# Kernel optimization log

Hardware: AMD Instinct MI355X
Metric: run time of the kernel (lower is better)

The kernel has to match this reference:

```python
import jax, jax.numpy as jnp
import numpy as np

D_MODEL = 1024
N_EXPERTS = 8
TOP_K = 2


def setup_inputs() -> dict:
    key = jax.random.key(0)
    ks = jax.random.split(key, 8)
    B, S, D, E, H = 4, 2048, D_MODEL, N_EXPERTS, 4 * D_MODEL
    s1 = 1.0 / np.sqrt(D)
    s2 = 1.0 / np.sqrt(H)
    return {
        "x": jax.random.normal(ks[0], (B, S, D), dtype=jnp.float32),
        "Wg": jax.random.uniform(ks[1], (D, E), jnp.float32, -s1, s1),
        "bg": jax.random.uniform(ks[2], (E,), jnp.float32, -s1, s1),
        "W1": jax.random.uniform(ks[3], (E, D, H), jnp.float32, -s1, s1),
        "b1": jax.random.uniform(ks[4], (E, H), jnp.float32, -s1, s1),
        "W2": jax.random.uniform(ks[5], (E, H, D), jnp.float32, -s2, s2),
        "b2": jax.random.uniform(ks[6], (E, D), jnp.float32, -s2, s2),
    }


def reference(x, Wg, bg, W1, b1, W2, b2):
    B, S, D = x.shape
    E = Wg.shape[1]
    x_flat = x.reshape(-1, D)                      # [T, D]
    logits = x_flat @ Wg + bg                      # [T, E]
    weights = jax.nn.softmax(logits, axis=-1)
    topk_w, topk_idx = jax.lax.top_k(weights, TOP_K)  # [T, K]
    # Per-token combine weight for each expert (sum over k where routed).
    onehot = jax.nn.one_hot(topk_idx, E, dtype=x.dtype)      # [T, K, E]
    combine = jnp.einsum("tk,tke->te", topk_w, onehot)       # [T, E]
    out = jnp.zeros_like(x_flat)
    for e in range(E):  # small fixed loop over experts
        h = jax.nn.gelu(x_flat @ W1[e] + b1[e], approximate=False)
        out = out + combine[:, e:e + 1] * (h @ W2[e] + b2[e])
    return out.reshape(B, S, D)
```

## Files before the change

### kernel.cpp

```cpp
#include <hip/hip_runtime.h>
#include <hip/hip_bf16.h>
#include <math.h>

#define T_TOK 8192
#define DM    1024
#define NE    8
#define HD    4096

typedef __bf16 bf16;
typedef __attribute__((ext_vector_type(8))) __bf16 bf16x8;
typedef __attribute__((ext_vector_type(4))) __bf16 bf16x4;
typedef __attribute__((ext_vector_type(4))) float  f32x4;

__device__ __forceinline__ void gl_lds16(const void* g, void* l) {
  __builtin_amdgcn_global_load_lds((const __attribute__((address_space(1))) void*)g,
                                   (__attribute__((address_space(3))) void*)l, 16, 0, 0);
}

#define RAW_BARRIER() asm volatile("s_barrier" ::: "memory")
#define WAIT_VM4()    asm volatile("s_waitcnt vmcnt(4)" ::: "memory")

__device__ __forceinline__ int imin(int a, int b) { return a < b ? a : b; }

__global__ void zero_kernel(float* __restrict__ out, int* __restrict__ counts) {
  size_t stride = (size_t)gridDim.x * blockDim.x;
  size_t n4 = (size_t)T_TOK * DM / 4;
  for (size_t i = (size_t)blockIdx.x * blockDim.x + threadIdx.x; i < n4; i += stride) {
    float4 z = {0.f, 0.f, 0.f, 0.f};
    ((float4*)out)[i] = z;
  }
  if (blockIdx.x == 0 && threadIdx.x < NE) counts[threadIdx.x] = 0;
}

__global__ void cvt_x_kernel(const float* __restrict__ x, bf16* __restrict__ xb) {
  size_t stride = (size_t)gridDim.x * blockDim.x;
  size_t n4 = (size_t)T_TOK * DM / 4;
  for (size_t i = (size_t)blockIdx.x * blockDim.x + threadIdx.x; i < n4; i += stride) {
    float4 v = ((const float4*)x)[i];
    bf16x4 o;
    o[0] = (bf16)v.x; o[1] = (bf16)v.y; o[2] = (bf16)v.z; o[3] = (bf16)v.w;
    *(bf16x4*)(xb + 4 * i) = o;
  }
}

__global__ void transpose_cvt_kernel(const float* __restrict__ in, bf16* __restrict__ out,
                                     int R, int C) {
  __shared__ float tile[64][65];
  int e = blockIdx.z;
  int c0 = blockIdx.x * 64, r0 = blockIdx.y * 64;
  int tid = threadIdx.x;
  int lr = tid >> 2, lc = (tid & 3) * 16;
  const float* src = in + ((size_t)e * R + r0 + lr) * C + c0 + lc;
#pragma unroll
  for (int q = 0; q < 4; ++q) {
    float4 v = *(const float4*)(src + q * 4);
    tile[lr][lc + q * 4 + 0] = v.x;
    tile[lr][lc + q * 4 + 1] = v.y;
    tile[lr][lc + q * 4 + 2] = v.z;
    tile[lr][lc + q * 4 + 3] = v.w;
  }
  __syncthreads();
  int oc = tid >> 3;
  int rchunk = tid & 7;
#pragma unroll
  for (int q = 0; q < 2; ++q) {
    int ocq = oc + q * 32;
    bf16x8 o;
#pragma unroll
    for (int k = 0; k < 8; ++k) o[k] = (bf16)tile[rchunk * 8 + k][ocq];
    *(bf16x8*)(out + ((size_t)e * C + c0 + ocq) * R + r0 + rchunk * 8) = o;
  }
}

__global__ void gating_kernel(const float* __restrict__ x, const float* __restrict__ Wg,
                              const float* __restrict__ bg, int* __restrict__ counts,
                              int* __restrict__ tokl, float* __restrict__ wgt) {
  int t = blockIdx.x * 4 + (threadIdx.x >> 6);
  int lane = threadIdx.x & 63;
  if (t >= T_TOK) return;
  double acc[NE];
#pragma unroll
  for (int e = 0; e < NE; ++e) acc[e] = 0.0;
  const float* xr = x + (size_t)t * DM;
  for (int d = lane; d < DM; d += 64) {
    float xv = xr[d];
#pragma unroll
    for (int e = 0; e < NE; ++e) acc[e] += (double)xv * (double)Wg[d * NE + e];
  }
#pragma unroll
  for (int e = 0; e < NE; ++e)
    for (int o = 32; o > 0; o >>= 1) acc[e] += __shfl_down(acc[e], o, 64);
  if (lane == 0) {
    float l[NE], w[NE];
    float m = -1e30f;
#pragma unroll
    for (int e = 0; e < NE; ++e) { l[e] = (float)acc[e] + bg[e]; m = fmaxf(m, l[e]); }
    float s = 0.f;
#pragma unroll
    for (int e = 0; e < NE; ++e) { w[e] = expf(l[e] - m); s += w[e]; }
    float inv = 1.f / s;
#pragma unroll
    for (int e = 0; e < NE; ++e) w[e] *= inv;
    int e1 = 0; float v1 = w[0];
#pragma unroll
    for (int e = 1; e < NE; ++e) if (w[e] > v1) { v1 = w[e]; e1 = e; }
    int e2 = -1; float v2 = -1.f;
#pragma unroll
    for (int e = 0; e < NE; ++e) if (e != e1 && w[e] > v2) { v2 = w[e]; e2 = e; }
    int s1 = atomicAdd(&counts[e1], 1);
    tokl[e1 * T_TOK + s1] = t; wgt[e1 * T_TOK + s1] = v1;
    int s2 = atomicAdd(&counts[e2], 1);
    tokl[e2 * T_TOK + s2] = t; wgt[e2 * T_TOK + s2] = v2;
  }
}

__global__ void scan_kernel(const int* __restrict__ counts, int* __restrict__ offsets) {
  if (threadIdx.x == 0 && blockIdx.x == 0) {
    int s = 0;
#pragma unroll
    for (int e = 0; e < NE; ++e) { offsets[e] = s; s += counts[e]; }
    offsets[NE] = s;
  }
}

__global__ __launch_bounds__(256, 3) void gemm1_kernel(
    const bf16* __restrict__ xbf, const bf16* __restrict__ w1t,
    const float* __restrict__ b1, const int* __restrict__ counts,
    const int* __restrict__ offsets, const int* __restrict__ tokl,
    bf16* __restrict__ hbuf, int Hc, int cbase) {
  int bid = blockIdx.x;
  int e = bid % NE;
  int pe = bid / NE;
  int NT = Hc / 128;
  int nt = pe % NT, rt = pe / NT;
  int cnt = counts[e];
  if (rt * 128 >= cnt) return;
  __shared__ __align__(16) bf16 sA[2][128 * 32];
  __shared__ __align__(16) bf16 sB[2][128 * 32];
  int tid = threadIdx.x, lane = tid & 63, w = tid >> 6;
  int slot = w * 2048 + lane * 16;
  int ra0 = slot >> 6, ko = slot & 63;
  int hoff = offsets[e];
  int r0 = imin(rt * 128 + ra0, cnt - 1);
  int r1 = imin(rt * 128 + ra0 + 16, cnt - 1);
  int t0 = tokl[e * T_TOK + r0];
  int t1 = tokl[e * T_TOK + r1];
  const char* ga0 = (const char*)(xbf + (size_t)t0 * DM) + ko;
  const char* ga1 = (const char*)(xbf + (size_t)t1 * DM) + ko;
  const char* gb0 = (const char*)(w1t + ((size_t)e * HD + cbase + nt * 128 + ra0) * DM) + ko;
  const char* gb1 = (const char*)(w1t + ((size_t)e * HD + cbase + nt * 128 + ra0 + 16) * DM) + ko;
  char* lab = (char*)sA + w * 2048;
  char* lbb = (char*)sB + w * 2048;
  f32x4 acc[4][4];
#pragma unroll
  for (int i = 0; i < 4; ++i)
#pragma unroll
    for (int j = 0; j < 4; ++j) acc[i][j] = {0.f, 0.f, 0.f, 0.f};
  int mw = (w & 1) * 64, nw = (w >> 1) * 64;
  const bf16* pa = &sA[0][0] + (size_t)(mw + (lane & 15)) * 32 + (lane >> 4) * 8;
  const bf16* pb = &sB[0][0] + (size_t)(nw + (lane & 15)) * 32 + (lane >> 4) * 8;
  const int K = DM / 32;
  gl_lds16(ga0, lab);
  gl_lds16(ga1, lab + 1024);
  gl_lds16(gb0, lbb);
  gl_lds16(gb1, lbb + 1024);
  for (int k = 0; k < K; ++k) {
    int nb = (k + 1) & 1;
    int kb = (k + 1 < K) ? (k + 1) * 64 : 0;
    gl_lds16(ga0 + kb, lab + nb * 8192);
    gl_lds16(ga1 + kb, lab + nb * 8192 + 1024);
    gl_lds16(gb0 + kb, lbb + nb * 8192);
    gl_lds16(gb1 + kb, lbb + nb * 8192 + 1024);
    WAIT_VM4();
    RAW_BARRIER();
    int cb = (k & 1) * 4096;
    bf16x8 af[4], bfr[4];
#pragma unroll
    for (int i = 0; i < 4; ++i) af[i] = *(const bf16x8*)(pa + cb + i * 16 * 32);
#pragma unroll
    for (int j = 0; j < 4; ++j) bfr[j] = *(const bf16x8*)(pb + cb + j * 16 * 32);
#pragma unroll
    for (int i = 0; i < 4; ++i)
#pragma unroll
      for (int j = 0; j < 4; ++j)
        acc[i][j] = __builtin_amdgcn_mfma_f32_16x16x32_bf16(af[i], bfr[j], acc[i][j], 0, 0, 0);
    RAW_BARRIER();
  }
  int colq = lane & 15, rowq = (lane >> 4) * 4;
  float b1v[4];
#pragma unroll
  for (int j = 0; j < 4; ++j)
    b1v[j] = b1[(size_t)e * HD + cbase + nt * 128 + nw + j * 16 + colq];
#pragma unroll
  for (int i = 0; i < 4; ++i) {
#pragma unroll
    for (int r = 0; r < 4; ++r) {
      int grow = rt * 128 + mw + i * 16 + rowq + r;
      if (grow < cnt) {
        size_t hrow = (size_t)(hoff + grow) * Hc;
#pragma unroll
        for (int j = 0; j < 4; ++j) {
          float v = acc[i][j][r] + b1v[j];
          float g = 0.5f * v * (1.f + erff(v * 0.70710678118654752f));
          hbuf[hrow + nt * 128 + nw + j * 16 + colq] = (bf16)g;
        }
      }
    }
  }
}

__global__ __launch_bounds__(256, 3) void gemm2_kernel(
    const bf16* __restrict__ hbuf, const bf16* __restrict__ w2t,
    const float* __restrict__ b2, const int* __restrict__ counts,
    const int* __restrict__ offsets, const int* __restrict__ tokl,
    const float* __restrict__ wgt, float* __restrict__ out,
    int Hc, int cbase, float b2scale) {
  int bid = blockIdx.x;
  int e = bid % NE;
  int pe = bid / NE;
  const int NT = DM / 128;
  int nt = pe % NT, rt = pe / NT;
  int cnt = counts[e];
  if (rt * 128 >= cnt) return;
  __shared__ __align__(16) bf16 sA[2][128 * 32];
  __shared__ __align__(16) bf16 sB[2][128 * 32];
  int tid = threadIdx.x, lane = tid & 63, w = tid >> 6;
  int slot = w * 2048 + lane * 16;
  int ra0 = slot >> 6, ko = slot & 63;
  int hoff = offsets[e];
  int r0 = imin(rt * 128 + ra0, cnt - 1);
  int r1 = imin(rt * 128 + ra0 + 16, cnt - 1);
  const char* ga0 = (const char*)(hbuf + (size_t)(hoff + r0) * Hc) + ko;
  const char* ga1 = (const char*)(hbuf + (size_t)(hoff + r1) * Hc) + ko;
  const char* gb0 = (const char*)(w2t + ((size_t)e * DM + nt * 128 + ra0) * HD + cbase) + ko;
  const char* gb1 = (const char*)(w2t + ((size_t)e * DM + nt * 128 + ra0 + 16) * HD + cbase) + ko;
  char* lab = (char*)sA + w * 2048;
  char* lbb = (char*)sB + w * 2048;
  f32x4 acc[4][4];
#pragma unroll
  for (int i = 0; i < 4; ++i)
#pragma unroll
    for (int j = 0; j < 4; ++j) acc[i][j] = {0.f, 0.f, 0.f, 0.f};
  int mw = (w & 1) * 64, nw = (w >> 1) * 64;
  const bf16* pa = &sA[0][0] + (size_t)(mw + (lane & 15)) * 32 + (lane >> 4) * 8;
  const bf16* pb = &sB[0][0] + (size_t)(nw + (lane & 15)) * 32 + (lane >> 4) * 8;
  const int K = Hc / 32;
  gl_lds16(ga0, lab);
  gl_lds16(ga1, lab + 1024);
  gl_lds16(gb0, lbb);
  gl_lds16(gb1, lbb + 1024);
  for (int k = 0; k < K; ++k) {
    int nb = (k + 1) & 1;
    int kb = (k + 1 < K) ? (k + 1) * 64 : 0;
    gl_lds16(ga0 + kb, lab + nb * 8192);
    gl_lds16(ga1 + kb, lab + nb * 8192 + 1024);
    gl_lds16(gb0 + kb, lbb + nb * 8192);
    gl_lds16(gb1 + kb, lbb + nb * 8192 + 1024);
    WAIT_VM4();
    RAW_BARRIER();
    int cb = (k & 1) * 4096;
    bf16x8 af[4], bfr[4];
#pragma unroll
    for (int i = 0; i < 4; ++i) af[i] = *(const bf16x8*)(pa + cb + i * 16 * 32);
#pragma unroll
    for (int j = 0; j < 4; ++j) bfr[j] = *(const bf16x8*)(pb + cb + j * 16 * 32);
#pragma unroll
    for (int i = 0; i < 4; ++i)
#pragma unroll
      for (int j = 0; j < 4; ++j)
        acc[i][j] = __builtin_amdgcn_mfma_f32_16x16x32_bf16(af[i], bfr[j], acc[i][j], 0, 0, 0);
    RAW_BARRIER();
  }
  int colq = lane & 15, rowq = (lane >> 4) * 4;
  float b2v[4];
#pragma unroll
  for (int j = 0; j < 4; ++j)
    b2v[j] = b2[(size_t)e * DM + nt * 128 + nw + j * 16 + colq] * b2scale;
#pragma unroll
  for (int i = 0; i < 4; ++i) {
#pragma unroll
    for (int r = 0; r < 4; ++r) {
      int grow = rt * 128 + mw + i * 16 + rowq + r;
      if (grow < cnt) {
        float wv = wgt[e * T_TOK + grow];
        int tk = tokl[e * T_TOK + grow];
        float* orow = out + (size_t)tk * DM + nt * 128 + nw;
#pragma unroll
        for (int j = 0; j < 4; ++j)
          atomicAdd(orow + j * 16 + colq, wv * (acc[i][j][r] + b2v[j]));
      }
    }
  }
}

extern "C" void kernel_launch(void* const* d_in, const int* in_sizes, int n_in,
                              void* d_out, int out_size, void* d_ws, size_t ws_size,
                              hipStream_t stream) {
  const float* x  = (const float*)d_in[0];
  const float* Wg = (const float*)d_in[1];
  const float* bg = (const float*)d_in[2];
  const float* W1 = (const float*)d_in[3];
  const float* b1 = (const float*)d_in[4];
  const float* W2 = (const float*)d_in[5];
  const float* b2 = (const float*)d_in[6];
  float* out = (float*)d_out;

  char* ws = (char*)d_ws;
  size_t off = 0;
  auto alloc = [&](size_t bytes) -> void* {
    void* p = ws + off;
    off = (off + bytes + 255) & ~(size_t)255;
    return p;
  };
  int*   counts  = (int*)alloc(NE * 4);
  int*   offsets = (int*)alloc((NE + 1) * 4);
  int*   tokl    = (int*)alloc((size_t)NE * T_TOK * 4);
  float* wgt     = (float*)alloc((size_t)NE * T_TOK * 4);
  bf16*  xbf     = (bf16*)alloc((size_t)T_TOK * DM * 2);
  bf16*  w1t     = (bf16*)alloc((size_t)NE * HD * DM * 2);
  bf16*  w2t     = (bf16*)alloc((size_t)NE * DM * HD * 2);
  size_t remain = ws_size > off ? ws_size - off : 0;
  int Hc = HD;
  while (Hc > 128 && (size_t)2 * T_TOK * Hc * 2 > remain) Hc >>= 1;
  bf16* hbuf = (bf16*)alloc((size_t)2 * T_TOK * Hc * 2);

  zero_kernel<<<4096, 256, 0, stream>>>(out, counts);
  cvt_x_kernel<<<2048, 256, 0, stream>>>(x, xbf);
  transpose_cvt_kernel<<<dim3(HD / 64, DM / 64, NE), 256, 0, stream>>>(W1, w1t, DM, HD);
  transpose_cvt_kernel<<<dim3(DM / 64, HD / 64, NE), 256, 0, stream>>>(W2, w2t, HD, DM);
  gating_kernel<<<T_TOK / 4, 256, 0, stream>>>(x, Wg, bg, counts, tokl, wgt);
  scan_kernel<<<1, 64, 0, stream>>>(counts, offsets);

  int nchunk = HD / Hc;
  for (int c = 0; c < nchunk; ++c) {
    gemm1_kernel<<<NE * (Hc / 128) * (T_TOK / 128), 256, 0, stream>>>(
        xbf, w1t, b1, counts, offsets, tokl, hbuf, Hc, c * Hc);
    gemm2_kernel<<<NE * (DM / 128) * (T_TOK / 128), 256, 0, stream>>>(
        hbuf, w2t, b2, counts, offsets, tokl, wgt, out, Hc, c * Hc, c == 0 ? 1.f : 0.f);
  }
}
```

Before: 1.007 ms.

## Enlarge expert GEMM tiles to 256x256x64 with swizzled LDS and fuse x conversion

Both grouped expert GEMMs move from 128x128 tiles with K-step 32 and 256 threads to 256x256 tiles with K-step 64 and 512 threads. LDS gets an XOR swizzle to avoid bank conflicts, and the block index is remapped so neighbouring blocks share an expert. The aim is more data reuse per byte loaded and fewer barriers per unit of MFMA work. The bf16 conversion of x moves into the gating kernel, removing one launch and one pass over x. The cost is heavier register and LDS use, 128 KB of LDS per block, which may limit occupancy, plus more padding waste on partial row tiles.

```diff
diff --git a/kernel.cpp b/kernel.cpp
--- a/kernel.cpp
+++ b/kernel.cpp
@@ -9,7 +9,6 @@
 
 typedef __bf16 bf16;
 typedef __attribute__((ext_vector_type(8))) __bf16 bf16x8;
-typedef __attribute__((ext_vector_type(4))) __bf16 bf16x4;
 typedef __attribute__((ext_vector_type(4))) float  f32x4;
 
 __device__ __forceinline__ void gl_lds16(const void* g, void* l) {
@@ -18,7 +17,7 @@
 }
 
 #define RAW_BARRIER() asm volatile("s_barrier" ::: "memory")
-#define WAIT_VM4()    asm volatile("s_waitcnt vmcnt(4)" ::: "memory")
+#define WAIT_VM8()    asm volatile("s_waitcnt vmcnt(8)" ::: "memory")
 
 __device__ __forceinline__ int imin(int a, int b) { return a < b ? a : b; }
 
@@ -30,17 +29,6 @@
     ((float4*)out)[i] = z;
   }
   if (blockIdx.x == 0 && threadIdx.x < NE) counts[threadIdx.x] = 0;
-}
-
-__global__ void cvt_x_kernel(const float* __restrict__ x, bf16* __restrict__ xb) {
-  size_t stride = (size_t)gridDim.x * blockDim.x;
-  size_t n4 = (size_t)T_TOK * DM / 4;
-  for (size_t i = (size_t)blockIdx.x * blockDim.x + threadIdx.x; i < n4; i += stride) {
-    float4 v = ((const float4*)x)[i];
-    bf16x4 o;
-    o[0] = (bf16)v.x; o[1] = (bf16)v.y; o[2] = (bf16)v.z; o[3] = (bf16)v.w;
-    *(bf16x4*)(xb + 4 * i) = o;
-  }
 }
 
 __global__ void transpose_cvt_kernel(const float* __restrict__ in, bf16* __restrict__ out,
@@ -74,7 +62,8 @@
 
 __global__ void gating_kernel(const float* __restrict__ x, const float* __restrict__ Wg,
                               const float* __restrict__ bg, int* __restrict__ counts,
-                              int* __restrict__ tokl, float* __restrict__ wgt) {
+                              int* __restrict__ tokl, float* __restrict__ wgt,
+                              bf16* __restrict__ xb) {
   int t = blockIdx.x * 4 + (threadIdx.x >> 6);
   int lane = threadIdx.x & 63;
   if (t >= T_TOK) return;
@@ -82,8 +71,10 @@
 #pragma unroll
   for (int e = 0; e < NE; ++e) acc[e] = 0.0;
   const float* xr = x + (size_t)t * DM;
+  bf16* xbr = xb + (size_t)t * DM;
   for (int d = lane; d < DM; d += 64) {
     float xv = xr[d];
+    xbr[d] = (bf16)xv;
 #pragma unroll
     for (int e = 0; e < NE; ++e) acc[e] += (double)xv * (double)Wg[d * NE + e];
   }
@@ -123,149 +114,194 @@
   }
 }
 
-__global__ __launch_bounds__(256, 3) void gemm1_kernel(
+
+__global__ __launch_bounds__(512, 2) void gemm1_kernel(
     const bf16* __restrict__ xbf, const bf16* __restrict__ w1t,
     const float* __restrict__ b1, const int* __restrict__ counts,
     const int* __restrict__ offsets, const int* __restrict__ tokl,
     bf16* __restrict__ hbuf, int Hc, int cbase) {
   int bid = blockIdx.x;
-  int e = bid % NE;
-  int pe = bid / NE;
-  int NT = Hc / 128;
-  int nt = pe % NT, rt = pe / NT;
+  int q = gridDim.x >> 3;
+  int L = (bid & 7) * q + (bid >> 3);
+  int rt = L & 31;
+  int g = L >> 5;
+  int NT = Hc >> 8;
+  int nt = g % NT, e = g / NT;
   int cnt = counts[e];
-  if (rt * 128 >= cnt) return;
-  __shared__ __align__(16) bf16 sA[2][128 * 32];
-  __shared__ __align__(16) bf16 sB[2][128 * 32];
+  if (rt * 256 >= cnt) return;
+  __shared__ __align__(16) bf16 sA[2][256 * 64];
+  __shared__ __align__(16) bf16 sB[2][256 * 64];
   int tid = threadIdx.x, lane = tid & 63, w = tid >> 6;
-  int slot = w * 2048 + lane * 16;
-  int ra0 = slot >> 6, ko = slot & 63;
+  int ra = tid >> 3;
+  int ko = (tid & 7) * 16;
+  int kox = ko ^ ((ra & 7) << 4);
   int hoff = offsets[e];
-  int r0 = imin(rt * 128 + ra0, cnt - 1);
-  int r1 = imin(rt * 128 + ra0 + 16, cnt - 1);
-  int t0 = tokl[e * T_TOK + r0];
-  int t1 = tokl[e * T_TOK + r1];
-  const char* ga0 = (const char*)(xbf + (size_t)t0 * DM) + ko;
-  const char* ga1 = (const char*)(xbf + (size_t)t1 * DM) + ko;
-  const char* gb0 = (const char*)(w1t + ((size_t)e * HD + cbase + nt * 128 + ra0) * DM) + ko;
-  const char* gb1 = (const char*)(w1t + ((size_t)e * HD + cbase + nt * 128 + ra0 + 16) * DM) + ko;
-  char* lab = (char*)sA + w * 2048;
-  char* lbb = (char*)sB + w * 2048;
-  f32x4 acc[4][4];
-#pragma unroll
-  for (int i = 0; i < 4; ++i)
+  const char* gA[4];
+  const char* gB[4];
+#pragma unroll
+  for (int s = 0; s < 4; ++s) {
+    int r = imin(rt * 256 + ra + s * 64, cnt - 1);
+    int t = tokl[e * T_TOK + r];
+    gA[s] = (const char*)(xbf + (size_t)t * DM) + kox;
+    int col = cbase + nt * 256 + ra + s * 64;
+    gB[s] = (const char*)(w1t + ((size_t)e * HD + col) * DM) + kox;
+  }
+  char* la = (char*)sA;
+  char* lb = (char*)sB;
+  int dst = w * 1024;
+  f32x4 acc[8][4];
+#pragma unroll
+  for (int i = 0; i < 8; ++i)
 #pragma unroll
     for (int j = 0; j < 4; ++j) acc[i][j] = {0.f, 0.f, 0.f, 0.f};
-  int mw = (w & 1) * 64, nw = (w >> 1) * 64;
-  const bf16* pa = &sA[0][0] + (size_t)(mw + (lane & 15)) * 32 + (lane >> 4) * 8;
-  const bf16* pb = &sB[0][0] + (size_t)(nw + (lane & 15)) * 32 + (lane >> 4) * 8;
-  const int K = DM / 32;
-  gl_lds16(ga0, lab);
-  gl_lds16(ga1, lab + 1024);
-  gl_lds16(gb0, lbb);
-  gl_lds16(gb1, lbb + 1024);
+  int mw = (w & 1) * 128, nw = (w >> 1) * 64;
+  int swzr = (lane & 7) << 4;
+  int colx = ((lane >> 4) * 16) ^ swzr;
+  const char* pa0 = (const char*)sA + (mw + (lane & 15)) * 128 + colx;
+  const char* pb0 = (const char*)sB + (nw + (lane & 15)) * 128 + colx;
+  const char* pa1 = (const char*)sA + (mw + (lane & 15)) * 128 + (colx ^ 64);
+  const char* pb1 = (const char*)sB + (nw + (lane & 15)) * 128 + (colx ^ 64);
+  const int K = DM / 64;
+#pragma unroll
+  for (int s = 0; s < 4; ++s) gl_lds16(gA[s], la + s * 8192 + dst);
+#pragma unroll
+  for (int s = 0; s < 4; ++s) gl_lds16(gB[s], lb + s * 8192 + dst);
   for (int k = 0; k < K; ++k) {
     int nb = (k + 1) & 1;
-    int kb = (k + 1 < K) ? (k + 1) * 64 : 0;
-    gl_lds16(ga0 + kb, lab + nb * 8192);
-    gl_lds16(ga1 + kb, lab + nb * 8192 + 1024);
-    gl_lds16(gb0 + kb, lbb + nb * 8192);
-    gl_lds16(gb1 + kb, lbb + nb * 8192 + 1024);
-    WAIT_VM4();
+    int kb = (k + 1 < K) ? (k + 1) * 128 : 0;
+    char* lan = la + nb * 32768;
+    char* lbn = lb + nb * 32768;
+#pragma unroll
+    for (int s = 0; s < 4; ++s) gl_lds16(gA[s] + kb, lan + s * 8192 + dst);
+#pragma unroll
+    for (int s = 0; s < 4; ++s) gl_lds16(gB[s] + kb, lbn + s * 8192 + dst);
+    WAIT_VM8();
     RAW_BARRIER();
-    int cb = (k & 1) * 4096;
-    bf16x8 af[4], bfr[4];
-#pragma unroll
-    for (int i = 0; i < 4; ++i) af[i] = *(const bf16x8*)(pa + cb + i * 16 * 32);
-#pragma unroll
-    for (int j = 0; j < 4; ++j) bfr[j] = *(const bf16x8*)(pb + cb + j * 16 * 32);
-#pragma unroll
-    for (int i = 0; i < 4; ++i)
+    int cb = (k & 1) * 32768;
+    bf16x8 af[8], bfr[4];
+#pragma unroll
+    for (int i = 0; i < 8; ++i) af[i] = *(const bf16x8*)(pa0 + cb + i * 2048);
+#pragma unroll
+    for (int j = 0; j < 4; ++j) bfr[j] = *(const bf16x8*)(pb0 + cb + j * 2048);
+#pragma unroll
+    for (int i = 0; i < 8; ++i)
+#pragma unroll
+      for (int j = 0; j < 4; ++j)
+        acc[i][j] = __builtin_amdgcn_mfma_f32_16x16x32_bf16(af[i], bfr[j], acc[i][j], 0, 0, 0);
+#pragma unroll
+    for (int i = 0; i < 8; ++i) af[i] = *(const bf16x8*)(pa1 + cb + i * 2048);
+#pragma unroll
+    for (int j = 0; j < 4; ++j) bfr[j] = *(const bf16x8*)(pb1 + cb + j * 2048);
+#pragma unroll
+    for (int i = 0; i < 8; ++i)
 #pragma unroll
       for (int j = 0; j < 4; ++j)
         acc[i][j] = __builtin_amdgcn_mfma_f32_16x16x32_bf16(af[i], bfr[j], acc[i][j], 0, 0, 0);
     RAW_BARRIER();
   }
   int colq = lane & 15, rowq = (lane >> 4) * 4;
+  int hcol = nt * 256 + nw;
   float b1v[4];
 #pragma unroll
   for (int j = 0; j < 4; ++j)
-    b1v[j] = b1[(size_t)e * HD + cbase + nt * 128 + nw + j * 16 + colq];
-#pragma unroll
-  for (int i = 0; i < 4; ++i) {
+    b1v[j] = b1[(size_t)e * HD + cbase + hcol + j * 16 + colq];
+#pragma unroll
+  for (int i = 0; i < 8; ++i) {
 #pragma unroll
     for (int r = 0; r < 4; ++r) {
-      int grow = rt * 128 + mw + i * 16 + rowq + r;
+      int grow = rt * 256 + mw + i * 16 + rowq + r;
       if (grow < cnt) {
         size_t hrow = (size_t)(hoff + grow) * Hc;
 #pragma unroll
         for (int j = 0; j < 4; ++j) {
           float v = acc[i][j][r] + b1v[j];
-          float g = 0.5f * v * (1.f + erff(v * 0.70710678118654752f));
-          hbuf[hrow + nt * 128 + nw + j * 16 + colq] = (bf16)g;
+          float gl = 0.5f * v * (1.f + erff(v * 0.70710678118654752f));
+          hbuf[hrow + hcol + j * 16 + colq] = (bf16)gl;
         }
       }
     }
   }
 }
 
-__global__ __launch_bounds__(256, 3) void gemm2_kernel(
+__global__ __launch_bounds__(512, 2) void gemm2_kernel(
     const bf16* __restrict__ hbuf, const bf16* __restrict__ w2t,
     const float* __restrict__ b2, const int* __restrict__ counts,
     const int* __restrict__ offsets, const int* __restrict__ tokl,
     const float* __restrict__ wgt, float* __restrict__ out,
     int Hc, int cbase, float b2scale) {
   int bid = blockIdx.x;
-  int e = bid % NE;
-  int pe = bid / NE;
-  const int NT = DM / 128;
-  int nt = pe % NT, rt = pe / NT;
+  int q = gridDim.x >> 3;
+  int L = (bid & 7) * q + (bid >> 3);
+  int rt = L & 31;
+  int g = L >> 5;
+  const int NT = DM / 256;
+  int nt = g % NT, e = g / NT;
   int cnt = counts[e];
-  if (rt * 128 >= cnt) return;
-  __shared__ __align__(16) bf16 sA[2][128 * 32];
-  __shared__ __align__(16) bf16 sB[2][128 * 32];
+  if (rt * 256 >= cnt) return;
+  __shared__ __align__(16) bf16 sA[2][256 * 64];
+  __shared__ __align__(16) bf16 sB[2][256 * 64];
   int tid = threadIdx.x, lane = tid & 63, w = tid >> 6;
-  int slot = w * 2048 + lane * 16;
-  int ra0 = slot >> 6, ko = slot & 63;
+  int ra = tid >> 3;
+  int ko = (tid & 7) * 16;
+  int kox = ko ^ ((ra & 7) << 4);
   int hoff = offsets[e];
-  int r0 = imin(rt * 128 + ra0, cnt - 1);
-  int r1 = imin(rt * 128 + ra0 + 16, cnt - 1);
-  const char* ga0 = (const char*)(hbuf + (size_t)(hoff + r0) * Hc) + ko;
-  const char* ga1 = (const char*)(hbuf + (size_t)(hoff + r1) * Hc) + ko;
-  const char* gb0 = (const char*)(w2t + ((size_t)e * DM + nt * 128 + ra0) * HD + cbase) + ko;
-  const char* gb1 = (const char*)(w2t + ((size_t)e * DM + nt * 128 + ra0 + 16) * HD + cbase) + ko;
-  char* lab = (char*)sA + w * 2048;
-  char* lbb = (char*)sB + w * 2048;
-  f32x4 acc[4][4];
-#pragma unroll
-  for (int i = 0; i < 4; ++i)
+  const char* gA[4];
+  const char* gB[4];
+#pragma unroll
+  for (int s = 0; s < 4; ++s) {
+    int r = imin(rt * 256 + ra + s * 64, cnt - 1);
+    gA[s] = (const char*)(hbuf + (size_t)(hoff + r) * Hc) + kox;
+    int col = nt * 256 + ra + s * 64;
+    gB[s] = (const char*)(w2t + ((size_t)e * DM + col) * HD + cbase) + kox;
+  }
+  char* la = (char*)sA;
+  char* lb = (char*)sB;
+  int dst = w * 1024;
+  f32x4 acc[8][4];
+#pragma unroll
+  for (int i = 0; i < 8; ++i)
 #pragma unroll
     for (int j = 0; j < 4; ++j) acc[i][j] = {0.f, 0.f, 0.f, 0.f};
-  int mw = (w & 1) * 64, nw = (w >> 1) * 64;
-  const bf16* pa = &sA[0][0] + (size_t)(mw + (lane & 15)) * 32 + (lane >> 4) * 8;
-  const bf16* pb = &sB[0][0] + (size_t)(nw + (lane & 15)) * 32 + (lane >> 4) * 8;
-  const int K = Hc / 32;
-  gl_lds16(ga0, lab);
-  gl_lds16(ga1, lab + 1024);
-  gl_lds16(gb0, lbb);
-  gl_lds16(gb1, lbb + 1024);
+  int mw = (w & 1) * 128, nw = (w >> 1) * 64;
+  int swzr = (lane & 7) << 4;
+  int colx = ((lane >> 4) * 16) ^ swzr;
+  const char* pa0 = (const char*)sA + (mw + (lane & 15)) * 128 + colx;
+  const char* pb0 = (const char*)sB + (nw + (lane & 15)) * 128 + colx;
+  const char* pa1 = (const char*)sA + (mw + (lane & 15)) * 128 + (colx ^ 64);
+  const char* pb1 = (const char*)sB + (nw + (lane & 15)) * 128 + (colx ^ 64);
+  const int K = Hc / 64;
+#pragma unroll
+  for (int s = 0; s < 4; ++s) gl_lds16(gA[s], la + s * 8192 + dst);
+#pragma unroll
+  for (int s = 0; s < 4; ++s) gl_lds16(gB[s], lb + s * 8192 + dst);
   for (int k = 0; k < K; ++k) {
     int nb = (k + 1) & 1;
-    int kb = (k + 1 < K) ? (k + 1) * 64 : 0;
-    gl_lds16(ga0 + kb, lab + nb * 8192);
-    gl_lds16(ga1 + kb, lab + nb * 8192 + 1024);
-    gl_lds16(gb0 + kb, lbb + nb * 8192);
-    gl_lds16(gb1 + kb, lbb + nb * 8192 + 1024);
-    WAIT_VM4();
+    int kb = (k + 1 < K) ? (k + 1) * 128 : 0;
+    char* lan = la + nb * 32768;
+    char* lbn = lb + nb * 32768;
+#pragma unroll
+    for (int s = 0; s < 4; ++s) gl_lds16(gA[s] + kb, lan + s * 8192 + dst);
+#pragma unroll
+    for (int s = 0; s < 4; ++s) gl_lds16(gB[s] + kb, lbn + s * 8192 + dst);
+    WAIT_VM8();
     RAW_BARRIER();
-    int cb = (k & 1) * 4096;
-    bf16x8 af[4], bfr[4];
-#pragma unroll
-    for (int i = 0; i < 4; ++i) af[i] = *(const bf16x8*)(pa + cb + i * 16 * 32);
-#pragma unroll
-    for (int j = 0; j < 4; ++j) bfr[j] = *(const bf16x8*)(pb + cb + j * 16 * 32);
-#pragma unroll
-    for (int i = 0; i < 4; ++i)
+    int cb = (k & 1) * 32768;
+    bf16x8 af[8], bfr[4];
+#pragma unroll
+    for (int i = 0; i < 8; ++i) af[i] = *(const bf16x8*)(pa0 + cb + i * 2048);
+#pragma unroll
+    for (int j = 0; j < 4; ++j) bfr[j] = *(const bf16x8*)(pb0 + cb + j * 2048);
+#pragma unroll
+    for (int i = 0; i < 8; ++i)
+#pragma unroll
+      for (int j = 0; j < 4; ++j)
+        acc[i][j] = __builtin_amdgcn_mfma_f32_16x16x32_bf16(af[i], bfr[j], acc[i][j], 0, 0, 0);
+#pragma unroll
+    for (int i = 0; i < 8; ++i) af[i] = *(const bf16x8*)(pa1 + cb + i * 2048);
+#pragma unroll
+    for (int j = 0; j < 4; ++j) bfr[j] = *(const bf16x8*)(pb1 + cb + j * 2048);
+#pragma unroll
+    for (int i = 0; i < 8; ++i)
 #pragma unroll
       for (int j = 0; j < 4; ++j)
         acc[i][j] = __builtin_amdgcn_mfma_f32_16x16x32_bf16(af[i], bfr[j], acc[i][j], 0, 0, 0);
@@ -275,16 +311,16 @@
   float b2v[4];
 #pragma unroll
   for (int j = 0; j < 4; ++j)
-    b2v[j] = b2[(size_t)e * DM + nt * 128 + nw + j * 16 + colq] * b2scale;
-#pragma unroll
-  for (int i = 0; i < 4; ++i) {
+    b2v[j] = b2[(size_t)e * DM + nt * 256 + nw + j * 16 + colq] * b2scale;
+#pragma unroll
+  for (int i = 0; i < 8; ++i) {
 #pragma unroll
     for (int r = 0; r < 4; ++r) {
-      int grow = rt * 128 + mw + i * 16 + rowq + r;
+      int grow = rt * 256 + mw + i * 16 + rowq + r;
       if (grow < cnt) {
         float wv = wgt[e * T_TOK + grow];
         int tk = tokl[e * T_TOK + grow];
-        float* orow = out + (size_t)tk * DM + nt * 128 + nw;
+        float* orow = out + (size_t)tk * DM + nt * 256 + nw;
 #pragma unroll
         for (int j = 0; j < 4; ++j)
           atomicAdd(orow + j * 16 + colq, wv * (acc[i][j][r] + b2v[j]));
@@ -321,21 +357,20 @@
   bf16*  w2t     = (bf16*)alloc((size_t)NE * DM * HD * 2);
   size_t remain = ws_size > off ? ws_size - off : 0;
   int Hc = HD;
-  while (Hc > 128 && (size_t)2 * T_TOK * Hc * 2 > remain) Hc >>= 1;
+  while (Hc > 256 && (size_t)2 * T_TOK * Hc * 2 > remain) Hc >>= 1;
   bf16* hbuf = (bf16*)alloc((size_t)2 * T_TOK * Hc * 2);
 
   zero_kernel<<<4096, 256, 0, stream>>>(out, counts);
-  cvt_x_kernel<<<2048, 256, 0, stream>>>(x, xbf);
   transpose_cvt_kernel<<<dim3(HD / 64, DM / 64, NE), 256, 0, stream>>>(W1, w1t, DM, HD);
   transpose_cvt_kernel<<<dim3(DM / 64, HD / 64, NE), 256, 0, stream>>>(W2, w2t, HD, DM);
-  gating_kernel<<<T_TOK / 4, 256, 0, stream>>>(x, Wg, bg, counts, tokl, wgt);
+  gating_kernel<<<T_TOK / 4, 256, 0, stream>>>(x, Wg, bg, counts, tokl, wgt, xbf);
   scan_kernel<<<1, 64, 0, stream>>>(counts, offsets);
 
   int nchunk = HD / Hc;
   for (int c = 0; c < nchunk; ++c) {
-    gemm1_kernel<<<NE * (Hc / 128) * (T_TOK / 128), 256, 0, stream>>>(
+    gemm1_kernel<<<NE * (Hc / 256) * (T_TOK / 256), 512, 0, stream>>>(
         xbf, w1t, b1, counts, offsets, tokl, hbuf, Hc, c * Hc);
-    gemm2_kernel<<<NE * (DM / 128) * (T_TOK / 128), 256, 0, stream>>>(
+    gemm2_kernel<<<NE * (DM / 256) * (T_TOK / 256), 512, 0, stream>>>(
         hbuf, w2t, b2, counts, offsets, tokl, wgt, out, Hc, c * Hc, c == 0 ? 1.f : 0.f);
   }
 }
```

New measurement: 1.155 ms. 14.7% more time.
